# Kernel tuning notes

Hardware: AMD Instinct MI355X
Metric: run time of the kernel (lower is better)

## Reference

```python
import jax, jax.numpy as jnp
import numpy as np

INPUTSIZE = 40
K = 5          # kenrnal_size
STRIDE = 3
KN = 32        # kenrnal_num
LABEL_NODES = 50
BATCH = 64
SAMPLE_NUM = 4


def _build_model():
    """Replicates __init__/create_J_H: dense symmetric Ising coupling J and field H."""
    starts = np.arange(0, INPUTSIZE - K + 1, STRIDE)          # window starts (torch unfold)
    win = starts[:, None] + np.arange(K)                      # [P, K] pixel rows/cols per window
    P = win.shape[0]
    # image_idxs[p] = flattened pixel indices of patch p (row-major over H windows then W windows)
    image_idxs = (win[:, None, :, None] * INPUTSIZE + win[None, :, None, :]).reshape(P * P, K * K)
    cnn_idxs = np.tile(image_idxs, (KN, 1))                   # [cnn_n, K*K]
    cnn_flags = np.repeat(np.arange(KN), P * P)               # kernel id per cnn node

    img_n = INPUTSIZE * INPUTSIZE
    cnn_n = cnn_idxs.shape[0]
    out_n = LABEL_NODES
    N = img_n + cnn_n + out_n

    rng = np.random.default_rng(0)
    J_CNN = (rng.standard_normal((KN, K * K)) * 0.01).astype(np.float32)
    J_MLP = (rng.standard_normal((cnn_n, out_n)) * 0.01).astype(np.float32)
    H = np.concatenate([
        rng.standard_normal(img_n) * 0.01,
        np.zeros(cnn_n),
        rng.standard_normal(out_n) * 0.01,
    ]).astype(np.float32)

    J = np.zeros((N, N), np.float32)
    rows = img_n + np.repeat(np.arange(cnn_n), K * K)
    cols = cnn_idxs.reshape(-1)
    vals = J_CNN[cnn_flags].reshape(-1)
    J[rows, cols] = vals
    J[cols, rows] = vals
    J[img_n:img_n + cnn_n, img_n + cnn_n:] = J_MLP
    J[img_n + cnn_n:, img_n:img_n + cnn_n] = J_MLP.T

    # Graph is bipartite (edges only cnn<->img and cnn<->out): valid 2-coloring.
    group1 = np.arange(img_n, img_n + cnn_n, dtype=np.int64)                      # cnn nodes
    group0 = np.concatenate([np.arange(img_n, dtype=np.int64),
                             np.arange(img_n + cnn_n, N, dtype=np.int64)])        # img + output nodes
    return J, H, group0, group1


def setup_inputs() -> dict:
    J, H, group0, group1 = _build_model()
    key = jax.random.key(0)
    # create_m: random +/-1 spins
    m = jnp.where(jax.random.randint(key, (BATCH, J.shape[0]), 0, 2) == 0, -1.0, 1.0).astype(jnp.float32)
    return {
        "m": m,
        "J": jnp.asarray(J),
        "H": jnp.asarray(H),
        "group0": jnp.asarray(group0),
        "group1": jnp.asarray(group1),
        "sample_num": SAMPLE_NUM,
    }


def reference(m, J, H, group0, group1, sample_num):
    """construct(): sample_num sweeps of per-color-group Gibbs updates.
    Per group: I = J[idxs] @ m.T + H[idxs]; m[:, idxs] = sign(tanh(I) - U(-1,1)).
    """
    keys = jax.random.split(jax.random.key(1), int(sample_num))

    def sweep(m, k):
        k0, k1 = jax.random.split(k)
        for idxs, kk in ((group0, k0), (group1, k1)):
            I = m @ J[idxs].T + H[idxs]                       # [B, |group|]
            u = jax.random.uniform(kk, I.shape, dtype=I.dtype) * 2.0 - 1.0
            m = m.at[:, idxs].set(jnp.sign(jnp.tanh(I) - u))
        return m, None

    m, _ = jax.lax.scan(sweep, m, keys)
    return m


if __name__ == "__main__":
    out = reference(**setup_inputs())
    print(out.shape, out.dtype)
```

## Files before the change

### kernel.cpp

```cpp
#include <hip/hip_runtime.h>
#include <stdint.h>

#define NN     6258
#define IMG_N  1600
#define CNN_N  4608
#define OUT_N  50
#define BATCH  64
#define G0SZ   1650
#define G1SZ   4608
#define IMGW   40
#define NPATCH 12
#define NB     256

__host__ __device__ inline void tf2x32(uint32_t k0, uint32_t k1,
                                       uint32_t x0, uint32_t x1,
                                       uint32_t& o0, uint32_t& o1) {
    uint32_t ks[3] = {k0, k1, k0 ^ k1 ^ 0x1BD11BDAu};
    const int rotA[4] = {13, 15, 26, 6};
    const int rotB[4] = {17, 29, 16, 24};
    x0 += ks[0];
    x1 += ks[1];
#pragma unroll
    for (int i = 0; i < 5; ++i) {
        const int* rot = (i & 1) ? rotB : rotA;
#pragma unroll
        for (int j = 0; j < 4; ++j) {
            x0 += x1;
            x1 = (x1 << rot[j]) | (x1 >> (32 - rot[j]));
            x1 ^= x0;
        }
        x0 += ks[(i + 1) % 3];
        x1 += ks[(i + 2) % 3] + (uint32_t)(i + 1);
    }
    o0 = x0;
    o1 = x1;
}

__device__ inline float jax_uniform_pm1(uint32_t k0, uint32_t k1, uint32_t j) {
    uint32_t o0, o1;
    tf2x32(k0, k1, 0u, j, o0, o1);
    uint32_t bits = o0 ^ o1;
    float f = __uint_as_float((bits >> 9) | 0x3f800000u);
    return (f - 1.0f) * 2.0f - 1.0f;
}

__device__ inline float tanh_xla_f32(float x) {
    if (fabsf(x) < 0.0004f) return x;
    float xc = fminf(fmaxf(x, -9.0f), 9.0f);
    float x2 = __fmul_rn(xc, xc);
    float num = -2.76076847742355e-16f;
    num = __fadd_rn(__fmul_rn(num, x2), 2.00018790482477e-13f);
    num = __fadd_rn(__fmul_rn(num, x2), -8.60467152213735e-11f);
    num = __fadd_rn(__fmul_rn(num, x2), 5.12229709037114e-08f);
    num = __fadd_rn(__fmul_rn(num, x2), 1.48572235717979e-05f);
    num = __fadd_rn(__fmul_rn(num, x2), 6.37261928875436e-04f);
    num = __fadd_rn(__fmul_rn(num, x2), 4.89352455891786e-03f);
    num = __fmul_rn(num, xc);
    float den = 1.19825839466702e-06f;
    den = __fadd_rn(__fmul_rn(den, x2), 1.18534705686654e-04f);
    den = __fadd_rn(__fmul_rn(den, x2), 2.26843463243900e-03f);
    den = __fadd_rn(__fmul_rn(den, x2), 4.89352518554385e-03f);
    return __fdiv_rn(num, den);
}

__device__ inline float gibbs_decide(double acc, float h, float u) {
    float I32 = (float)(acc + (double)h);
    float t = tanh_xla_f32(I32);
    float d = __fadd_rn(t, -u);
    return (d > 0.0f) ? 1.0f : ((d < 0.0f) ? -1.0f : 0.0f);
}

struct SweepKeys { uint32_t v[16]; };

__global__ __launch_bounds__(256) void zinit(uint32_t* p) {
    p[threadIdx.x * 16] = 0u;
    if (threadIdx.x == 0) p[4096] = 0u;
}

__device__ __forceinline__ void grid_sync(uint32_t* flags, uint32_t* gen, uint32_t k) {
    __syncthreads();
    const int tid = (int)threadIdx.x;
    if (tid == 0)
        __hip_atomic_store(&flags[blockIdx.x * 16], k, __ATOMIC_RELEASE,
                           __HIP_MEMORY_SCOPE_AGENT);
    if (blockIdx.x == 0 && tid < 64) {
        for (;;) {
            bool mine = true;
#pragma unroll
            for (int i = 0; i < 4; ++i) {
                uint32_t v = __hip_atomic_load(&flags[(tid + i * 64) * 16],
                                               __ATOMIC_RELAXED, __HIP_MEMORY_SCOPE_AGENT);
                mine &= (v >= k);
            }
            if (__all(mine)) break;
            __builtin_amdgcn_s_sleep(1);
        }
        if (tid == 0)
            __hip_atomic_store(gen, k, __ATOMIC_RELEASE, __HIP_MEMORY_SCOPE_AGENT);
    }
    if (tid == 0) {
        while (__hip_atomic_load(gen, __ATOMIC_RELAXED, __HIP_MEMORY_SCOPE_AGENT) < k)
            __builtin_amdgcn_s_sleep(1);
        (void)__hip_atomic_load(gen, __ATOMIC_ACQUIRE, __HIP_MEMORY_SCOPE_AGENT);
    }
    __syncthreads();
}

__global__ __launch_bounds__(256) void fused(const float* __restrict__ m_in,
                                             const float* __restrict__ J,
                                             const float* __restrict__ H,
                                             float* __restrict__ m_out,
                                             float* __restrict__ mt,
                                             SweepKeys keys) {
    uint32_t* flags = (uint32_t*)m_out;
    uint32_t* gen   = flags + 4096;
    uint32_t  bk    = 0;
    __shared__ float  jc[800];
    __shared__ double red[4][64];
    const int tid  = (int)threadIdx.x;
    const int blk  = (int)blockIdx.x;
    const int lane = tid & 63;
    const int wave = tid >> 6;
    const int gwid = blk * 4 + wave;

    for (int t = blk * 256 + tid; t < NN * BATCH; t += NB * 256)
        mt[t] = m_in[(size_t)(t & 63) * NN + (t >> 6)];
    for (int t = tid; t < 800; t += 256) {
        int f = t / 25, pos = t % 25;
        jc[t] = J[(size_t)(IMG_N + f * 144) * NN + (pos / 5) * IMGW + (pos % 5)];
    }
    grid_sync(flags, gen, ++bk);

    for (int s = 0; s < 4; ++s) {
        const uint32_t k0a = keys.v[s * 4 + 0], k0b = keys.v[s * 4 + 1];
        const uint32_t k1a = keys.v[s * 4 + 2], k1b = keys.v[s * 4 + 3];

        if (blk < 50) {
            const int o = blk;
            const float* Jrow = J + (size_t)(IMG_N + CNN_N + o) * NN + IMG_N;
            double a0 = 0.0, a1 = 0.0;
            const int k0i = wave * 1152;
#pragma unroll 4
            for (int k = 0; k < 1152; k += 2) {
                a0 += (double)Jrow[k0i + k]     * (double)mt[(IMG_N + k0i + k) * 64 + lane];
                a1 += (double)Jrow[k0i + k + 1] * (double)mt[(IMG_N + k0i + k + 1) * 64 + lane];
            }
            red[wave][lane] = a0 + a1;
            __syncthreads();
            if (wave == 0) {
                double a = ((red[0][lane] + red[1][lane]) + red[2][lane]) + red[3][lane];
                float u = jax_uniform_pm1(k0a, k0b, (uint32_t)(lane * G0SZ + IMG_N + o));
                mt[(IMG_N + CNN_N + o) * 64 + lane] =
                    gibbs_decide(a, H[IMG_N + CNN_N + o], u);
            }
        } else {
            const int iw = (blk - 50) * 4 + wave;
            for (int g = iw; g < IMG_N; g += 824) {
                int r = g / IMGW, c = g % IMGW;
                int pr_lo = (r >= 4) ? (r - 2) / 3 : 0;
                int pr_hi = r / 3; if (pr_hi > NPATCH - 1) pr_hi = NPATCH - 1;
                int pc_lo = (c >= 4) ? (c - 2) / 3 : 0;
                int pc_hi = c / 3; if (pc_hi > NPATCH - 1) pc_hi = NPATCH - 1;
                double acc = 0.0;
                for (int pr = pr_lo; pr <= pr_hi; ++pr) {
                    for (int pc = pc_lo; pc <= pc_hi; ++pc) {
                        int pos = (r - 3 * pr) * 5 + (c - 3 * pc);
                        int node0 = IMG_N + pr * NPATCH + pc;
#pragma unroll
                        for (int f = 0; f < 32; ++f)
                            acc += (double)jc[f * 25 + pos] *
                                   (double)mt[(node0 + f * 144) * 64 + lane];
                    }
                }
                float u = jax_uniform_pm1(k0a, k0b, (uint32_t)(lane * G0SZ + g));
                mt[g * 64 + lane] = gibbs_decide(acc, H[g], u);
            }
        }
        grid_sync(flags, gen, ++bk);

        for (int cn = gwid; cn < CNN_N; cn += NB * 4) {
            int f = cn / 144;
            int p = cn - f * 144;
            int pr = p / NPATCH, pc = p - pr * NPATCH;
            int r0 = pr * 3, c0 = pc * 3;
            double acc = 0.0;
#pragma unroll
            for (int a = 0; a < 5; ++a) {
                int rowbase = (r0 + a) * IMGW + c0;
#pragma unroll
                for (int bb = 0; bb < 5; ++bb)
                    acc += (double)jc[f * 25 + a * 5 + bb] *
                           (double)mt[(rowbase + bb) * 64 + lane];
            }
            const float* Jo = J + (size_t)(IMG_N + cn) * NN + IMG_N + CNN_N;
#pragma unroll 10
            for (int o = 0; o < OUT_N; ++o)
                acc += (double)Jo[o] * (double)mt[(IMG_N + CNN_N + o) * 64 + lane];
            float u = jax_uniform_pm1(k1a, k1b, (uint32_t)(lane * G1SZ + cn));
            mt[(IMG_N + cn) * 64 + lane] = gibbs_decide(acc, H[IMG_N + cn], u);
        }
        grid_sync(flags, gen, ++bk);
    }

    for (int t = blk * 256 + tid; t < NN * BATCH; t += NB * 256) {
        int b = t / NN, node = t - b * NN;
        m_out[t] = mt[node * 64 + b];
    }
}

extern "C" void kernel_launch(void* const* d_in, const int* in_sizes, int n_in,
                              void* d_out, int out_size, void* d_ws, size_t ws_size,
                              hipStream_t stream) {
    const float* m_in = (const float*)d_in[0];
    const float* J    = (const float*)d_in[1];
    const float* H    = (const float*)d_in[2];
    float* m_out = (float*)d_out;
    float* mt    = (float*)d_ws;

    uint32_t K[4][2];
    for (int i = 0; i < 4; ++i)
        tf2x32(0u, 1u, 0u, (uint32_t)i, K[i][0], K[i][1]);
    SweepKeys keys;
    for (int s = 0; s < 4; ++s) {
        uint32_t k0a, k0b, k1a, k1b;
        tf2x32(K[s][0], K[s][1], 0u, 0u, k0a, k0b);
        tf2x32(K[s][0], K[s][1], 0u, 1u, k1a, k1b);
        keys.v[s * 4 + 0] = k0a; keys.v[s * 4 + 1] = k0b;
        keys.v[s * 4 + 2] = k1a; keys.v[s * 4 + 3] = k1b;
    }

    zinit<<<1, 256, 0, stream>>>((uint32_t*)d_out);
    fused<<<NB, 256, 0, stream>>>(m_in, J, H, m_out, mt, keys);
}
```

Before: 459.1 us.

## Quadruple grid to 1024 blocks, stage output spins in LDS, widen accumulators

Raises the persistent grid from 256 to 1024 blocks, so each wave handles a single image node and fewer CNN nodes per phase. The grid barrier is reworked so all 256 threads of block 0 poll the flags, and the flag and generation arrays are resized to match. The 50 output spins are copied into shared memory before the CNN phase so they are not re-read from global memory per node, and the output-node dot product uses four accumulators. The risk is that a 1024-block cooperative grid may not all be co-resident, which would deadlock the spin barrier, and barrier cost grows with block count.

```diff
diff --git a/kernel.cpp b/kernel.cpp
--- a/kernel.cpp
+++ b/kernel.cpp
@@ -10,7 +10,7 @@
 #define G1SZ   4608
 #define IMGW   40
 #define NPATCH 12
-#define NB     256
+#define NB     1024
 
 __host__ __device__ inline void tf2x32(uint32_t k0, uint32_t k1,
                                        uint32_t x0, uint32_t x1,
@@ -73,8 +73,8 @@
 struct SweepKeys { uint32_t v[16]; };
 
 __global__ __launch_bounds__(256) void zinit(uint32_t* p) {
-    p[threadIdx.x * 16] = 0u;
-    if (threadIdx.x == 0) p[4096] = 0u;
+    for (int t = (int)threadIdx.x; t < NB; t += 256) p[t * 16] = 0u;
+    if (threadIdx.x == 0) p[16384] = 0u;
 }
 
 __device__ __forceinline__ void grid_sync(uint32_t* flags, uint32_t* gen, uint32_t k) {
@@ -83,20 +83,19 @@
     if (tid == 0)
         __hip_atomic_store(&flags[blockIdx.x * 16], k, __ATOMIC_RELEASE,
                            __HIP_MEMORY_SCOPE_AGENT);
-    if (blockIdx.x == 0 && tid < 64) {
-        for (;;) {
-            bool mine = true;
-#pragma unroll
-            for (int i = 0; i < 4; ++i) {
-                uint32_t v = __hip_atomic_load(&flags[(tid + i * 64) * 16],
-                                               __ATOMIC_RELAXED, __HIP_MEMORY_SCOPE_AGENT);
-                mine &= (v >= k);
-            }
-            if (__all(mine)) break;
-            __builtin_amdgcn_s_sleep(1);
-        }
-        if (tid == 0)
+    if (blockIdx.x == 0) {
+#pragma unroll
+        for (int i = 0; i < 4; ++i) {
+            uint32_t* f = &flags[(tid + i * 256) * 16];
+            while (__hip_atomic_load(f, __ATOMIC_RELAXED, __HIP_MEMORY_SCOPE_AGENT) < k)
+                __builtin_amdgcn_s_sleep(1);
+        }
+        __syncthreads();
+        if (tid == 0) {
+            (void)__hip_atomic_load(&flags[0], __ATOMIC_ACQUIRE,
+                                    __HIP_MEMORY_SCOPE_AGENT);
             __hip_atomic_store(gen, k, __ATOMIC_RELEASE, __HIP_MEMORY_SCOPE_AGENT);
+        }
     }
     if (tid == 0) {
         while (__hip_atomic_load(gen, __ATOMIC_RELAXED, __HIP_MEMORY_SCOPE_AGENT) < k)
@@ -113,9 +112,10 @@
                                              float* __restrict__ mt,
                                              SweepKeys keys) {
     uint32_t* flags = (uint32_t*)m_out;
-    uint32_t* gen   = flags + 4096;
+    uint32_t* gen   = flags + 16384;
     uint32_t  bk    = 0;
     __shared__ float  jc[800];
+    __shared__ float  mo[OUT_N * 64];
     __shared__ double red[4][64];
     const int tid  = (int)threadIdx.x;
     const int blk  = (int)blockIdx.x;
@@ -138,14 +138,16 @@
         if (blk < 50) {
             const int o = blk;
             const float* Jrow = J + (size_t)(IMG_N + CNN_N + o) * NN + IMG_N;
-            double a0 = 0.0, a1 = 0.0;
+            double a0 = 0.0, a1 = 0.0, a2 = 0.0, a3 = 0.0;
             const int k0i = wave * 1152;
-#pragma unroll 4
-            for (int k = 0; k < 1152; k += 2) {
+#pragma unroll 2
+            for (int k = 0; k < 1152; k += 4) {
                 a0 += (double)Jrow[k0i + k]     * (double)mt[(IMG_N + k0i + k) * 64 + lane];
                 a1 += (double)Jrow[k0i + k + 1] * (double)mt[(IMG_N + k0i + k + 1) * 64 + lane];
-            }
-            red[wave][lane] = a0 + a1;
+                a2 += (double)Jrow[k0i + k + 2] * (double)mt[(IMG_N + k0i + k + 2) * 64 + lane];
+                a3 += (double)Jrow[k0i + k + 3] * (double)mt[(IMG_N + k0i + k + 3) * 64 + lane];
+            }
+            red[wave][lane] = (a0 + a1) + (a2 + a3);
             __syncthreads();
             if (wave == 0) {
                 double a = ((red[0][lane] + red[1][lane]) + red[2][lane]) + red[3][lane];
@@ -154,8 +156,8 @@
                     gibbs_decide(a, H[IMG_N + CNN_N + o], u);
             }
         } else {
-            const int iw = (blk - 50) * 4 + wave;
-            for (int g = iw; g < IMG_N; g += 824) {
+            const int g = (blk - 50) * 4 + wave;
+            if (g < IMG_N) {
                 int r = g / IMGW, c = g % IMGW;
                 int pr_lo = (r >= 4) ? (r - 2) / 3 : 0;
                 int pr_hi = r / 3; if (pr_hi > NPATCH - 1) pr_hi = NPATCH - 1;
@@ -178,6 +180,9 @@
         }
         grid_sync(flags, gen, ++bk);
 
+        for (int t = tid; t < OUT_N * 64; t += 256)
+            mo[t] = mt[(IMG_N + CNN_N) * 64 + t];
+        __syncthreads();
         for (int cn = gwid; cn < CNN_N; cn += NB * 4) {
             int f = cn / 144;
             int p = cn - f * 144;
@@ -195,7 +200,7 @@
             const float* Jo = J + (size_t)(IMG_N + cn) * NN + IMG_N + CNN_N;
 #pragma unroll 10
             for (int o = 0; o < OUT_N; ++o)
-                acc += (double)Jo[o] * (double)mt[(IMG_N + CNN_N + o) * 64 + lane];
+                acc += (double)Jo[o] * (double)mo[o * 64 + lane];
             float u = jax_uniform_pm1(k1a, k1b, (uint32_t)(lane * G1SZ + cn));
             mt[(IMG_N + cn) * 64 + lane] = gibbs_decide(acc, H[IMG_N + cn], u);
         }
```

New measurement: 606.3 us. +32.1%, slower.
